# Kernel optimization log

Measured on AMD Instinct MI355X. Metric: run time of the kernel, lower is better.

The kernel has to match this reference:

```python
import jax, jax.numpy as jnp
import numpy as np

HIDDEN = 2048
INTER = 768
NUM_EXPERTS = 32
TOP_K = 4
NUM_TOKENS = 2048


def setup_inputs() -> dict:
    key = jax.random.key(0)
    ks = jax.random.split(key, 5)
    scale = 0.02
    x = jax.random.normal(ks[0], (NUM_TOKENS, HIDDEN), dtype=jnp.float32)
    w_router = jax.random.normal(ks[1], (HIDDEN, NUM_EXPERTS), dtype=jnp.float32) * scale
    w_gate = jax.random.normal(ks[2], (NUM_EXPERTS, HIDDEN, INTER), dtype=jnp.float32) * scale
    w_up = jax.random.normal(ks[3], (NUM_EXPERTS, HIDDEN, INTER), dtype=jnp.float32) * scale
    w_down = jax.random.normal(ks[4], (NUM_EXPERTS, INTER, HIDDEN), dtype=jnp.float32) * scale
    return {"hidden_states": x, "w_router": w_router, "w_gate": w_gate,
            "w_up": w_up, "w_down": w_down}


def reference(hidden_states, w_router, w_gate, w_up, w_down):
    x = hidden_states  # [T, H]
    T = x.shape[0]
    # Router: softmax over experts (in input dtype), top-k, renormalize.
    router_logits = x @ w_router                      # [T, E]
    routing_weights = jax.nn.softmax(router_logits, axis=-1)
    top_w, top_idx = jax.lax.top_k(routing_weights, TOP_K)  # [T, K]
    top_w = top_w / jnp.sum(top_w, axis=-1, keepdims=True)   # norm_topk_prob
    # Dense combine weights: combine[t, e] = routing weight if expert e selected
    # for token t, else 0.  (top-k indices are unique per token.)
    combine = jnp.zeros((T, NUM_EXPERTS), dtype=x.dtype)
    combine = combine.at[jnp.arange(T)[:, None], top_idx].add(top_w)  # [T, E]

    # Scan over experts: each step computes one expert's SwiGLU MLP on all
    # tokens and accumulates it weighted by its combine weight (tokens with
    # zero weight contribute nothing, matching the gather/scatter original).
    def body(acc, expert):
        wg, wu, wd, cw = expert  # [H,I], [H,I], [I,H], [T]
        h = jax.nn.silu(x @ wg) * (x @ wu)   # [T, I]
        return acc + (h @ wd) * cw[:, None], None

    out, _ = jax.lax.scan(body, jnp.zeros_like(x),
                          (w_gate, w_up, w_down, combine.T))
    return out
```

## Files before the change

kernel.cpp:

```cpp
#include <hip/hip_runtime.h>

#define T_TOK 2048
#define HID   2048
#define INTER 768
#define NE    32
#define NSLOT 8192
#define MAXT  96

typedef short bf16x8 __attribute__((ext_vector_type(8)));
typedef float f32x4  __attribute__((ext_vector_type(4)));

__device__ __forceinline__ unsigned short f2b(float f){
  unsigned u = __builtin_bit_cast(unsigned, f);
  u += 0x7fffu + ((u >> 16) & 1u);
  return (unsigned short)(u >> 16);
}
__device__ __forceinline__ unsigned pk2(float a, float b){
  return (unsigned)f2b(a) | ((unsigned)f2b(b) << 16);
}

#define XB_OFF    0ul
#define HBUF_OFF  8388608ul
#define TKW_OFF   20971520ul
#define TKI_OFF   21004288ul
#define ROWS_OFF  21037056ul
#define WTS_OFF   21069824ul
#define OFFS_OFF  21102592ul
#define LOGIT_OFF 21102848ul
#define CNT_OFF   21364992ul
#define FILL_OFF  21365120ul
#define TLIST_OFF 21365248ul
#define ZERO_OFF  21102848ul
#define ZERO_SZ   (262144ul + 128ul + 128ul)

__global__ void convert_x_kernel(const float* __restrict__ x, ushort* __restrict__ xb){
  int i = (blockIdx.x * 256 + threadIdx.x) * 8;
  float4 a = *(const float4*)(x + i);
  float4 b = *(const float4*)(x + i + 4);
  uint4 o;
  o.x = pk2(a.x, a.y);
  o.y = pk2(a.z, a.w);
  o.z = pk2(b.x, b.y);
  o.w = pk2(b.z, b.w);
  *(uint4*)(xb + i) = o;
}

__global__ void router_gemm(const float* __restrict__ x, const float* __restrict__ wr,
                            float* __restrict__ logits){
  const int tt = blockIdx.x;
  const int kb = blockIdx.y;
  __shared__ float xs[64 * 64];
  __shared__ float wsm[64 * 32];
  const int tid = threadIdx.x;
  const int r = tid >> 5, e = tid & 31;
  float acc[8];
#pragma unroll
  for (int i = 0; i < 8; i++) acc[i] = 0.0f;

  for (int sub = 0; sub < 4; ++sub){
    const int k0 = kb * 256 + sub * 64;
    __syncthreads();
#pragma unroll
    for (int j = 0; j < 4; j++){
      int f4 = tid + j * 256;
      int row = f4 >> 4, c4 = f4 & 15;
      float4 v = *(const float4*)(x + (size_t)(tt * 64 + row) * HID + k0 + c4 * 4);
      *(float4*)(xs + row * 64 + c4 * 4) = v;
    }
#pragma unroll
    for (int j = 0; j < 2; j++){
      int f4 = tid + j * 256;
      int row = f4 >> 3, c4 = f4 & 7;
      float4 v = *(const float4*)(wr + (size_t)(k0 + row) * NE + c4 * 4);
      *(float4*)(wsm + row * NE + c4 * 4) = v;
    }
    __syncthreads();
    for (int kk = 0; kk < 64; kk++){
      float wv = wsm[kk * NE + e];
#pragma unroll
      for (int i = 0; i < 8; i++) acc[i] += xs[(r + i * 8) * 64 + kk] * wv;
    }
  }
#pragma unroll
  for (int i = 0; i < 8; i++)
    atomicAdd(&logits[(size_t)(tt * 64 + r + i * 8) * NE + e], acc[i]);
}

__global__ void topk_kernel(const float* __restrict__ logits, float* __restrict__ topk_w,
                            int* __restrict__ topk_i, int* __restrict__ counts){
  int t = blockIdx.x * blockDim.x + threadIdx.x;
  if (t >= T_TOK) return;
  float l[32];
  const float4* lp = (const float4*)(logits + (size_t)t * NE);
#pragma unroll
  for (int i = 0; i < 8; i++){
    float4 v = lp[i];
    l[i*4+0] = v.x; l[i*4+1] = v.y; l[i*4+2] = v.z; l[i*4+3] = v.w;
  }
  float m = l[0];
#pragma unroll
  for (int i = 1; i < 32; i++) m = fmaxf(m, l[i]);
#pragma unroll
  for (int i = 0; i < 32; i++) l[i] = __expf(l[i] - m);
  float wsel[4]; int isel[4];
#pragma unroll
  for (int k = 0; k < 4; k++){
    float best = l[0]; int bi = 0;
#pragma unroll
    for (int i = 1; i < 32; i++){ if (l[i] > best){ best = l[i]; bi = i; } }
    wsel[k] = best; isel[k] = bi; l[bi] = -1.0f;
  }
  float s4 = wsel[0] + wsel[1] + wsel[2] + wsel[3];
  float inv = 1.0f / s4;
#pragma unroll
  for (int k = 0; k < 4; k++){
    topk_w[t * 4 + k] = wsel[k] * inv;
    topk_i[t * 4 + k] = isel[k];
    atomicAdd(&counts[isel[k]], 1);
  }
}

__global__ void prefix_kernel(const int* __restrict__ counts, int* __restrict__ offsets,
                              int* __restrict__ tlist){
  if (threadIdx.x == 0){
    int a = 0; offsets[0] = 0; int nt_ = 0;
    for (int e = 0; e < NE; e++){
      int c = counts[e];
      for (int m = 0; m * 128 < c && nt_ < MAXT; m++) tlist[nt_++] = e | (m << 16);
      a += c; offsets[e + 1] = a;
    }
    for (; nt_ < MAXT; nt_++) tlist[nt_] = -1;
  }
}

__global__ void scatter_kernel(const int* __restrict__ topk_i, const float* __restrict__ topk_w,
                               const int* __restrict__ offsets, int* __restrict__ fill,
                               int* __restrict__ rows, float* __restrict__ wts){
  int gid = blockIdx.x * 256 + threadIdx.x;
  int t = gid >> 2;
  int e = topk_i[gid];
  int pos = atomicAdd(&fill[e], 1);
  int s = offsets[e] + pos;
  rows[s] = t;
  wts[s] = topk_w[gid];
}

#define NT_GU 32
__global__ __launch_bounds__(512, 2) void gateup_kernel(
    const ushort* __restrict__ xb, const float* __restrict__ wg,
    const float* __restrict__ wu, const int* __restrict__ rows,
    const float* __restrict__ wts, const int* __restrict__ counts,
    const int* __restrict__ offsets, const int* __restrict__ tlist,
    ushort* __restrict__ hbuf)
{
  const int w = tlist[blockIdx.y];
  if (w < 0) return;
  const int e = w & 0xffff, mt = w >> 16;
  const int nt = blockIdx.x;
  const int cnt = counts[e];
  const int off = offsets[e];
  const int n0 = nt * 64;

  __shared__ __align__(16) ushort lds[2 * 16384];

  const int tid = threadIdx.x;

  const int ra = tid >> 2, quad = tid & 3;
  const int srow = mt * 128 + ra;
  const int slotA = off + (srow < cnt ? srow : 0);
  const int tokA = rows[slotA];
  const ushort* agp = xb + (size_t)tokA * HID;
  const int q0 = quad * 2, q1 = q0 + 1;
  const int axk = ra & 7;
  const int adst0 = ra * 64 + (q0 ^ axk) * 8;
  const int adst1 = ra * 64 + (q1 ^ axk) * 8;

  const int bn = tid & 63, kg = tid >> 6;
  const size_t wofs = (size_t)e * (HID * INTER) + n0 + bn;
  const float* wgp = wg + wofs;
  const float* wup = wu + wofs;
  const int bdst = bn * 64 + (kg ^ (bn & 7)) * 8;

  const int lane = tid & 63, wv = tid >> 6;
  const int wm = wv >> 1, wn = wv & 1;
  const int fr = lane & 15, ko = lane >> 4;
  const int fxk = fr & 7;

  f32x4 accg[2][2], accu[2][2];
#pragma unroll
  for (int i = 0; i < 2; i++)
#pragma unroll
    for (int j = 0; j < 2; j++){ accg[i][j] = (f32x4)(0.0f); accu[i][j] = (f32x4)(0.0f); }

  uint4 pa0, pa1;
  float sg[8], su[8];

  pa0 = *(const uint4*)(agp + q0 * 8);
  pa1 = *(const uint4*)(agp + q1 * 8);
  {
    const float* pg_ = wgp + (size_t)(kg * 8) * INTER;
    const float* pu_ = wup + (size_t)(kg * 8) * INTER;
#pragma unroll
    for (int kk = 0; kk < 8; kk++){ sg[kk] = pg_[(size_t)kk * INTER]; su[kk] = pu_[(size_t)kk * INTER]; }
  }
  {
    ushort* dA = lds;
    *(uint4*)(dA + adst0) = pa0;
    *(uint4*)(dA + adst1) = pa1;
    uint4 pg, pu;
    pg.x = pk2(sg[0], sg[1]); pg.y = pk2(sg[2], sg[3]);
    pg.z = pk2(sg[4], sg[5]); pg.w = pk2(sg[6], sg[7]);
    pu.x = pk2(su[0], su[1]); pu.y = pk2(su[2], su[3]);
    pu.z = pk2(su[4], su[5]); pu.w = pk2(su[6], su[7]);
    *(uint4*)(dA + 8192 + bdst) = pg;
    *(uint4*)(dA + 12288 + bdst) = pu;
  }
  __syncthreads();

  int cbase = 0;
  for (int t = 0; t < NT_GU; ++t){
    const int nb = cbase ^ 16384;
    if (t + 1 < NT_GU){
      const int k0 = (t + 1) * 64;
      pa0 = *(const uint4*)(agp + k0 + q0 * 8);
      pa1 = *(const uint4*)(agp + k0 + q1 * 8);
      const float* pg_ = wgp + (size_t)(k0 + kg * 8) * INTER;
      const float* pu_ = wup + (size_t)(k0 + kg * 8) * INTER;
#pragma unroll
      for (int kk = 0; kk < 8; kk++){ sg[kk] = pg_[(size_t)kk * INTER]; su[kk] = pu_[(size_t)kk * INTER]; }
    }
    const ushort* A  = lds + cbase;
    const ushort* BG = lds + cbase + 8192;
    const ushort* BU = lds + cbase + 12288;
#pragma unroll
    for (int kk = 0; kk < 2; kk++){
      const int bsel = ((kk * 4 + ko) ^ fxk) * 8;
      bf16x8 a[2], bg2[2], bu2[2];
#pragma unroll
      for (int mf = 0; mf < 2; mf++)
        a[mf] = *(const bf16x8*)(A + (wm * 32 + mf * 16 + fr) * 64 + bsel);
#pragma unroll
      for (int nf = 0; nf < 2; nf++){
        bg2[nf] = *(const bf16x8*)(BG + (wn * 32 + nf * 16 + fr) * 64 + bsel);
        bu2[nf] = *(const bf16x8*)(BU + (wn * 32 + nf * 16 + fr) * 64 + bsel);
      }
#pragma unroll
      for (int mf = 0; mf < 2; mf++)
#pragma unroll
        for (int nf = 0; nf < 2; nf++){
          accg[mf][nf] = __builtin_amdgcn_mfma_f32_16x16x32_bf16(a[mf], bg2[nf], accg[mf][nf], 0, 0, 0);
          accu[mf][nf] = __builtin_amdgcn_mfma_f32_16x16x32_bf16(a[mf], bu2[nf], accu[mf][nf], 0, 0, 0);
        }
    }
    if (t + 1 < NT_GU){
      ushort* dA = lds + nb;
      *(uint4*)(dA + adst0) = pa0;
      *(uint4*)(dA + adst1) = pa1;
      uint4 pg, pu;
      pg.x = pk2(sg[0], sg[1]); pg.y = pk2(sg[2], sg[3]);
      pg.z = pk2(sg[4], sg[5]); pg.w = pk2(sg[6], sg[7]);
      pu.x = pk2(su[0], su[1]); pu.y = pk2(su[2], su[3]);
      pu.z = pk2(su[4], su[5]); pu.w = pk2(su[6], su[7]);
      *(uint4*)(dA + 8192 + bdst) = pg;
      *(uint4*)(dA + 12288 + bdst) = pu;
    }
    __syncthreads();
    cbase = nb;
  }

#pragma unroll
  for (int mf = 0; mf < 2; mf++)
#pragma unroll
    for (int j = 0; j < 4; j++){
      int rl = wm * 32 + mf * 16 + ko * 4 + j;
      int gr = mt * 128 + rl;
      if (gr < cnt){
        float w2 = wts[off + gr];
        size_t robase = (size_t)(off + gr) * INTER + n0;
#pragma unroll
        for (int nf = 0; nf < 2; nf++){
          float g = accg[mf][nf][j], u = accu[mf][nf][j];
          float h = (g / (1.0f + __expf(-g))) * u * w2;
          hbuf[robase + wn * 32 + nf * 16 + fr] = f2b(h);
        }
      }
    }
}

#define NT_DN 12
__global__ __launch_bounds__(512, 2) void down_kernel(
    const ushort* __restrict__ hbuf, const float* __restrict__ wd,
    const int* __restrict__ rows, const int* __restrict__ counts,
    const int* __restrict__ offsets, const int* __restrict__ tlist,
    float* __restrict__ out)
{
  const int w = tlist[blockIdx.y];
  if (w < 0) return;
  const int e = w & 0xffff, mt = w >> 16;
  const int nt = blockIdx.x;
  const int cnt = counts[e];
  const int off = offsets[e];
  const int n0 = nt * 64;

  __shared__ __align__(16) ushort lds[2 * 12288];

  const int tid = threadIdx.x;

  const int ra = tid >> 2, quad = tid & 3;
  const int srow = mt * 128 + ra;
  const int slotA = off + (srow < cnt ? srow : 0);
  const ushort* agp = hbuf + (size_t)slotA * INTER;
  const int q0 = quad * 2, q1 = q0 + 1;
  const int axk = ra & 7;
  const int adst0 = ra * 64 + (q0 ^ axk) * 8;
  const int adst1 = ra * 64 + (q1 ^ axk) * 8;

  const int bn = tid & 63, kg = tid >> 6;
  const float* wdp = wd + (size_t)e * (INTER * HID) + n0 + bn;
  const int bdst = bn * 64 + (kg ^ (bn & 7)) * 8;

  const int lane = tid & 63, wv = tid >> 6;
  const int wm = wv >> 1, wn = wv & 1;
  const int fr = lane & 15, ko = lane >> 4;
  const int fxk = fr & 7;

  f32x4 acc[2][2];
#pragma unroll
  for (int i = 0; i < 2; i++)
#pragma unroll
    for (int j = 0; j < 2; j++) acc[i][j] = (f32x4)(0.0f);

  uint4 pa0, pa1;
  float sb[8];

  pa0 = *(const uint4*)(agp + q0 * 8);
  pa1 = *(const uint4*)(agp + q1 * 8);
  {
    const float* p = wdp + (size_t)(kg * 8) * HID;
#pragma unroll
    for (int kk = 0; kk < 8; kk++) sb[kk] = p[(size_t)kk * HID];
  }
  {
    ushort* dA = lds;
    *(uint4*)(dA + adst0) = pa0;
    *(uint4*)(dA + adst1) = pa1;
    uint4 pb;
    pb.x = pk2(sb[0], sb[1]); pb.y = pk2(sb[2], sb[3]);
    pb.z = pk2(sb[4], sb[5]); pb.w = pk2(sb[6], sb[7]);
    *(uint4*)(dA + 8192 + bdst) = pb;
  }
  __syncthreads();

  int cbase = 0;
  for (int t = 0; t < NT_DN; ++t){
    const int nb = cbase ^ 12288;
    if (t + 1 < NT_DN){
      const int k0 = (t + 1) * 64;
      pa0 = *(const uint4*)(agp + k0 + q0 * 8);
      pa1 = *(const uint4*)(agp + k0 + q1 * 8);
      const float* p = wdp + (size_t)(k0 + kg * 8) * HID;
#pragma unroll
      for (int kk = 0; kk < 8; kk++) sb[kk] = p[(size_t)kk * HID];
    }
    const ushort* A = lds + cbase;
    const ushort* B = lds + cbase + 8192;
#pragma unroll
    for (int kk = 0; kk < 2; kk++){
      const int bsel = ((kk * 4 + ko) ^ fxk) * 8;
      bf16x8 a[2], b2[2];
#pragma unroll
      for (int mf = 0; mf < 2; mf++)
        a[mf] = *(const bf16x8*)(A + (wm * 32 + mf * 16 + fr) * 64 + bsel);
#pragma unroll
      for (int nf = 0; nf < 2; nf++)
        b2[nf] = *(const bf16x8*)(B + (wn * 32 + nf * 16 + fr) * 64 + bsel);
#pragma unroll
      for (int mf = 0; mf < 2; mf++)
#pragma unroll
        for (int nf = 0; nf < 2; nf++)
          acc[mf][nf] = __builtin_amdgcn_mfma_f32_16x16x32_bf16(a[mf], b2[nf], acc[mf][nf], 0, 0, 0);
    }
    if (t + 1 < NT_DN){
      ushort* dA = lds + nb;
      *(uint4*)(dA + adst0) = pa0;
      *(uint4*)(dA + adst1) = pa1;
      uint4 pb;
      pb.x = pk2(sb[0], sb[1]); pb.y = pk2(sb[2], sb[3]);
      pb.z = pk2(sb[4], sb[5]); pb.w = pk2(sb[6], sb[7]);
      *(uint4*)(dA + 8192 + bdst) = pb;
    }
    __syncthreads();
    cbase = nb;
  }

#pragma unroll
  for (int mf = 0; mf < 2; mf++)
#pragma unroll
    for (int j = 0; j < 4; j++){
      int rl = wm * 32 + mf * 16 + ko * 4 + j;
      int gr = mt * 128 + rl;
      if (gr < cnt){
        int tok = rows[off + gr];
        float* obase = out + (size_t)tok * HID + n0;
#pragma unroll
        for (int nf = 0; nf < 2; nf++)
          atomicAdd(obase + wn * 32 + nf * 16 + fr, acc[mf][nf][j]);
      }
    }
}

extern "C" void kernel_launch(void* const* d_in, const int* in_sizes, int n_in,
                              void* d_out, int out_size, void* d_ws, size_t ws_size,
                              hipStream_t stream){
  const float* x  = (const float*)d_in[0];
  const float* wr = (const float*)d_in[1];
  const float* wg = (const float*)d_in[2];
  const float* wu = (const float*)d_in[3];
  const float* wd = (const float*)d_in[4];
  float* out = (float*)d_out;
  char* ws = (char*)d_ws;

  ushort* xb     = (ushort*)(ws + XB_OFF);
  ushort* hbuf   = (ushort*)(ws + HBUF_OFF);
  float*  topkw  = (float*)(ws + TKW_OFF);
  int*    topki  = (int*)(ws + TKI_OFF);
  int*    rows   = (int*)(ws + ROWS_OFF);
  float*  wts    = (float*)(ws + WTS_OFF);
  int*    offs   = (int*)(ws + OFFS_OFF);
  float*  logits = (float*)(ws + LOGIT_OFF);
  int*    counts = (int*)(ws + CNT_OFF);
  int*    fill   = (int*)(ws + FILL_OFF);
  int*    tlist  = (int*)(ws + TLIST_OFF);

  hipMemsetAsync(ws + ZERO_OFF, 0, ZERO_SZ, stream);
  hipMemsetAsync(d_out, 0, (size_t)out_size * sizeof(float), stream);

  convert_x_kernel<<<2048, 256, 0, stream>>>(x, xb);
  router_gemm<<<dim3(32, 8), 256, 0, stream>>>(x, wr, logits);
  topk_kernel<<<8, 256, 0, stream>>>(logits, topkw, topki, counts);
  prefix_kernel<<<1, 64, 0, stream>>>(counts, offs, tlist);
  scatter_kernel<<<32, 256, 0, stream>>>(topki, topkw, offs, fill, rows, wts);
  gateup_kernel<<<dim3(12, MAXT), 512, 0, stream>>>(xb, wg, wu, rows, wts, counts, offs, tlist, hbuf);
  down_kernel<<<dim3(32, MAXT), 512, 0, stream>>>(hbuf, wd, rows, counts, offs, tlist, out);
}
```

Before: 347.7 us.

## Deepen prefetch, swap grid order, replace output atomics with slot buffer plus combine

Both GEMM kernels now hold two register prefetch sets, unrolling the double-buffered loop by two so global loads run two tiles ahead. The launch-bounds occupancy hint rises from 2 to 4 and the grid axes are swapped so the expert/m-tile index varies fastest. When the workspace is large enough, the down projection writes per-slot fp32 rows instead of atomically adding into the output, and a new combine kernel sums each token's four slots. This removes atomics and the output memset at the cost of a 64MB intermediate buffer and extra memory traffic, and the tighter register budget risks spills.

```diff
diff --git a/kernel.cpp b/kernel.cpp
--- a/kernel.cpp
+++ b/kernel.cpp
@@ -30,6 +30,9 @@
 #define CNT_OFF   21364992ul
 #define FILL_OFF  21365120ul
 #define TLIST_OFF 21365248ul
+#define T2S_OFF   21365760ul
+#define HB2_OFF   21398528ul
+#define WS_NEED   (HB2_OFF + 67108864ul)
 #define ZERO_OFF  21102848ul
 #define ZERO_SZ   (262144ul + 128ul + 128ul)
 
@@ -135,7 +138,8 @@
 
 __global__ void scatter_kernel(const int* __restrict__ topk_i, const float* __restrict__ topk_w,
                                const int* __restrict__ offsets, int* __restrict__ fill,
-                               int* __restrict__ rows, float* __restrict__ wts){
+                               int* __restrict__ rows, float* __restrict__ wts,
+                               int* __restrict__ t2s){
   int gid = blockIdx.x * 256 + threadIdx.x;
   int t = gid >> 2;
   int e = topk_i[gid];
@@ -143,20 +147,21 @@
   int s = offsets[e] + pos;
   rows[s] = t;
   wts[s] = topk_w[gid];
+  t2s[gid] = s;
 }
 
 #define NT_GU 32
-__global__ __launch_bounds__(512, 2) void gateup_kernel(
+__global__ __launch_bounds__(512, 4) void gateup_kernel(
     const ushort* __restrict__ xb, const float* __restrict__ wg,
     const float* __restrict__ wu, const int* __restrict__ rows,
     const float* __restrict__ wts, const int* __restrict__ counts,
     const int* __restrict__ offsets, const int* __restrict__ tlist,
     ushort* __restrict__ hbuf)
 {
-  const int w = tlist[blockIdx.y];
+  const int w = tlist[blockIdx.x];
   if (w < 0) return;
   const int e = w & 0xffff, mt = w >> 16;
-  const int nt = blockIdx.x;
+  const int nt = blockIdx.y;
   const int cnt = counts[e];
   const int off = offsets[e];
   const int n0 = nt * 64;
@@ -192,46 +197,33 @@
 #pragma unroll
     for (int j = 0; j < 2; j++){ accg[i][j] = (f32x4)(0.0f); accu[i][j] = (f32x4)(0.0f); }
 
-  uint4 pa0, pa1;
-  float sg[8], su[8];
-
-  pa0 = *(const uint4*)(agp + q0 * 8);
-  pa1 = *(const uint4*)(agp + q1 * 8);
-  {
-    const float* pg_ = wgp + (size_t)(kg * 8) * INTER;
-    const float* pu_ = wup + (size_t)(kg * 8) * INTER;
-#pragma unroll
-    for (int kk = 0; kk < 8; kk++){ sg[kk] = pg_[(size_t)kk * INTER]; su[kk] = pu_[(size_t)kk * INTER]; }
-  }
-  {
-    ushort* dA = lds;
-    *(uint4*)(dA + adst0) = pa0;
-    *(uint4*)(dA + adst1) = pa1;
+  uint4 A0a, A0b, A1a, A1b;
+  float G0[8], U0[8], G1[8], U1[8];
+
+  auto loadSet = [&](int k0, uint4 &aa, uint4 &ab, float *g, float *u){
+    aa = *(const uint4*)(agp + k0 + q0 * 8);
+    ab = *(const uint4*)(agp + k0 + q1 * 8);
+    const float* pg_ = wgp + (size_t)(k0 + kg * 8) * INTER;
+    const float* pu_ = wup + (size_t)(k0 + kg * 8) * INTER;
+#pragma unroll
+    for (int kk = 0; kk < 8; kk++){ g[kk] = pg_[(size_t)kk * INTER]; u[kk] = pu_[(size_t)kk * INTER]; }
+  };
+  auto writeSet = [&](int base, uint4 aa, uint4 ab, const float *g, const float *u){
+    ushort* dA = lds + base;
+    *(uint4*)(dA + adst0) = aa;
+    *(uint4*)(dA + adst1) = ab;
     uint4 pg, pu;
-    pg.x = pk2(sg[0], sg[1]); pg.y = pk2(sg[2], sg[3]);
-    pg.z = pk2(sg[4], sg[5]); pg.w = pk2(sg[6], sg[7]);
-    pu.x = pk2(su[0], su[1]); pu.y = pk2(su[2], su[3]);
-    pu.z = pk2(su[4], su[5]); pu.w = pk2(su[6], su[7]);
+    pg.x = pk2(g[0], g[1]); pg.y = pk2(g[2], g[3]);
+    pg.z = pk2(g[4], g[5]); pg.w = pk2(g[6], g[7]);
+    pu.x = pk2(u[0], u[1]); pu.y = pk2(u[2], u[3]);
+    pu.z = pk2(u[4], u[5]); pu.w = pk2(u[6], u[7]);
     *(uint4*)(dA + 8192 + bdst) = pg;
     *(uint4*)(dA + 12288 + bdst) = pu;
-  }
-  __syncthreads();
-
-  int cbase = 0;
-  for (int t = 0; t < NT_GU; ++t){
-    const int nb = cbase ^ 16384;
-    if (t + 1 < NT_GU){
-      const int k0 = (t + 1) * 64;
-      pa0 = *(const uint4*)(agp + k0 + q0 * 8);
-      pa1 = *(const uint4*)(agp + k0 + q1 * 8);
-      const float* pg_ = wgp + (size_t)(k0 + kg * 8) * INTER;
-      const float* pu_ = wup + (size_t)(k0 + kg * 8) * INTER;
-#pragma unroll
-      for (int kk = 0; kk < 8; kk++){ sg[kk] = pg_[(size_t)kk * INTER]; su[kk] = pu_[(size_t)kk * INTER]; }
-    }
-    const ushort* A  = lds + cbase;
-    const ushort* BG = lds + cbase + 8192;
-    const ushort* BU = lds + cbase + 12288;
+  };
+  auto computeTile = [&](int base){
+    const ushort* A  = lds + base;
+    const ushort* BG = lds + base + 8192;
+    const ushort* BU = lds + base + 12288;
 #pragma unroll
     for (int kk = 0; kk < 2; kk++){
       const int bsel = ((kk * 4 + ko) ^ fxk) * 8;
@@ -252,20 +244,22 @@
           accu[mf][nf] = __builtin_amdgcn_mfma_f32_16x16x32_bf16(a[mf], bu2[nf], accu[mf][nf], 0, 0, 0);
         }
     }
-    if (t + 1 < NT_GU){
-      ushort* dA = lds + nb;
-      *(uint4*)(dA + adst0) = pa0;
-      *(uint4*)(dA + adst1) = pa1;
-      uint4 pg, pu;
-      pg.x = pk2(sg[0], sg[1]); pg.y = pk2(sg[2], sg[3]);
-      pg.z = pk2(sg[4], sg[5]); pg.w = pk2(sg[6], sg[7]);
-      pu.x = pk2(su[0], su[1]); pu.y = pk2(su[2], su[3]);
-      pu.z = pk2(su[4], su[5]); pu.w = pk2(su[6], su[7]);
-      *(uint4*)(dA + 8192 + bdst) = pg;
-      *(uint4*)(dA + 12288 + bdst) = pu;
-    }
-    __syncthreads();
-    cbase = nb;
+  };
+
+  loadSet(0,  A0a, A0b, G0, U0);
+  loadSet(64, A1a, A1b, G1, U1);
+  writeSet(0, A0a, A0b, G0, U0);
+  __syncthreads();
+
+  for (int t = 0; t < NT_GU; t += 2){
+    if (t + 2 < NT_GU) loadSet((t + 2) * 64, A0a, A0b, G0, U0);
+    computeTile(0);
+    writeSet(16384, A1a, A1b, G1, U1);
+    __syncthreads();
+    if (t + 3 < NT_GU) loadSet((t + 3) * 64, A1a, A1b, G1, U1);
+    computeTile(16384);
+    if (t + 2 < NT_GU) writeSet(0, A0a, A0b, G0, U0);
+    __syncthreads();
   }
 
 #pragma unroll
@@ -288,16 +282,17 @@
 }
 
 #define NT_DN 12
-__global__ __launch_bounds__(512, 2) void down_kernel(
+template<bool SLOT>
+__global__ __launch_bounds__(512, 4) void down_kernel(
     const ushort* __restrict__ hbuf, const float* __restrict__ wd,
     const int* __restrict__ rows, const int* __restrict__ counts,
     const int* __restrict__ offsets, const int* __restrict__ tlist,
-    float* __restrict__ out)
+    float* __restrict__ outp)
 {
-  const int w = tlist[blockIdx.y];
+  const int w = tlist[blockIdx.x];
   if (w < 0) return;
   const int e = w & 0xffff, mt = w >> 16;
-  const int nt = blockIdx.x;
+  const int nt = blockIdx.y;
   const int cnt = counts[e];
   const int off = offsets[e];
   const int n0 = nt * 64;
@@ -330,40 +325,28 @@
 #pragma unroll
     for (int j = 0; j < 2; j++) acc[i][j] = (f32x4)(0.0f);
 
-  uint4 pa0, pa1;
-  float sb[8];
-
-  pa0 = *(const uint4*)(agp + q0 * 8);
-  pa1 = *(const uint4*)(agp + q1 * 8);
-  {
-    const float* p = wdp + (size_t)(kg * 8) * HID;
-#pragma unroll
-    for (int kk = 0; kk < 8; kk++) sb[kk] = p[(size_t)kk * HID];
-  }
-  {
-    ushort* dA = lds;
-    *(uint4*)(dA + adst0) = pa0;
-    *(uint4*)(dA + adst1) = pa1;
+  uint4 A0a, A0b, A1a, A1b;
+  float B0[8], B1[8];
+
+  auto loadSet = [&](int k0, uint4 &aa, uint4 &ab, float *b){
+    aa = *(const uint4*)(agp + k0 + q0 * 8);
+    ab = *(const uint4*)(agp + k0 + q1 * 8);
+    const float* p = wdp + (size_t)(k0 + kg * 8) * HID;
+#pragma unroll
+    for (int kk = 0; kk < 8; kk++) b[kk] = p[(size_t)kk * HID];
+  };
+  auto writeSet = [&](int base, uint4 aa, uint4 ab, const float *b){
+    ushort* dA = lds + base;
+    *(uint4*)(dA + adst0) = aa;
+    *(uint4*)(dA + adst1) = ab;
     uint4 pb;
-    pb.x = pk2(sb[0], sb[1]); pb.y = pk2(sb[2], sb[3]);
-    pb.z = pk2(sb[4], sb[5]); pb.w = pk2(sb[6], sb[7]);
+    pb.x = pk2(b[0], b[1]); pb.y = pk2(b[2], b[3]);
+    pb.z = pk2(b[4], b[5]); pb.w = pk2(b[6], b[7]);
     *(uint4*)(dA + 8192 + bdst) = pb;
-  }
-  __syncthreads();
-
-  int cbase = 0;
-  for (int t = 0; t < NT_DN; ++t){
-    const int nb = cbase ^ 12288;
-    if (t + 1 < NT_DN){
-      const int k0 = (t + 1) * 64;
-      pa0 = *(const uint4*)(agp + k0 + q0 * 8);
-      pa1 = *(const uint4*)(agp + k0 + q1 * 8);
-      const float* p = wdp + (size_t)(k0 + kg * 8) * HID;
-#pragma unroll
-      for (int kk = 0; kk < 8; kk++) sb[kk] = p[(size_t)kk * HID];
-    }
-    const ushort* A = lds + cbase;
-    const ushort* B = lds + cbase + 8192;
+  };
+  auto computeTile = [&](int base){
+    const ushort* A = lds + base;
+    const ushort* B = lds + base + 8192;
 #pragma unroll
     for (int kk = 0; kk < 2; kk++){
       const int bsel = ((kk * 4 + ko) ^ fxk) * 8;
@@ -380,17 +363,22 @@
         for (int nf = 0; nf < 2; nf++)
           acc[mf][nf] = __builtin_amdgcn_mfma_f32_16x16x32_bf16(a[mf], b2[nf], acc[mf][nf], 0, 0, 0);
     }
-    if (t + 1 < NT_DN){
-      ushort* dA = lds + nb;
-      *(uint4*)(dA + adst0) = pa0;
-      *(uint4*)(dA + adst1) = pa1;
-      uint4 pb;
-      pb.x = pk2(sb[0], sb[1]); pb.y = pk2(sb[2], sb[3]);
-      pb.z = pk2(sb[4], sb[5]); pb.w = pk2(sb[6], sb[7]);
-      *(uint4*)(dA + 8192 + bdst) = pb;
-    }
-    __syncthreads();
-    cbase = nb;
+  };
+
+  loadSet(0,  A0a, A0b, B0);
+  loadSet(64, A1a, A1b, B1);
+  writeSet(0, A0a, A0b, B0);
+  __syncthreads();
+
+  for (int t = 0; t < NT_DN; t += 2){
+    if (t + 2 < NT_DN) loadSet((t + 2) * 64, A0a, A0b, B0);
+    computeTile(0);
+    writeSet(12288, A1a, A1b, B1);
+    __syncthreads();
+    if (t + 3 < NT_DN) loadSet((t + 3) * 64, A1a, A1b, B1);
+    computeTile(12288);
+    if (t + 2 < NT_DN) writeSet(0, A0a, A0b, B0);
+    __syncthreads();
   }
 
 #pragma unroll
@@ -400,13 +388,38 @@
       int rl = wm * 32 + mf * 16 + ko * 4 + j;
       int gr = mt * 128 + rl;
       if (gr < cnt){
-        int tok = rows[off + gr];
-        float* obase = out + (size_t)tok * HID + n0;
-#pragma unroll
-        for (int nf = 0; nf < 2; nf++)
-          atomicAdd(obase + wn * 32 + nf * 16 + fr, acc[mf][nf][j]);
+        if (SLOT){
+          float* obase = outp + (size_t)(off + gr) * HID + n0;
+#pragma unroll
+          for (int nf = 0; nf < 2; nf++)
+            obase[wn * 32 + nf * 16 + fr] = acc[mf][nf][j];
+        } else {
+          int tok = rows[off + gr];
+          float* obase = outp + (size_t)tok * HID + n0;
+#pragma unroll
+          for (int nf = 0; nf < 2; nf++)
+            atomicAdd(obase + wn * 32 + nf * 16 + fr, acc[mf][nf][j]);
+        }
       }
     }
+}
+
+__global__ void combine_kernel(const float* __restrict__ hbuf2, const int* __restrict__ t2s,
+                               float* __restrict__ out){
+  const int t = blockIdx.y;
+  const int c4 = (blockIdx.x * 256 + threadIdx.x) * 4;
+  const int s0 = t2s[t * 4 + 0], s1 = t2s[t * 4 + 1];
+  const int s2 = t2s[t * 4 + 2], s3 = t2s[t * 4 + 3];
+  float4 a = *(const float4*)(hbuf2 + (size_t)s0 * HID + c4);
+  float4 b = *(const float4*)(hbuf2 + (size_t)s1 * HID + c4);
+  float4 c = *(const float4*)(hbuf2 + (size_t)s2 * HID + c4);
+  float4 d = *(const float4*)(hbuf2 + (size_t)s3 * HID + c4);
+  float4 r;
+  r.x = a.x + b.x + c.x + d.x;
+  r.y = a.y + b.y + c.y + d.y;
+  r.z = a.z + b.z + c.z + d.z;
+  r.w = a.w + b.w + c.w + d.w;
+  *(float4*)(out + (size_t)t * HID + c4) = r;
 }
 
 extern "C" void kernel_launch(void* const* d_in, const int* in_sizes, int n_in,
@@ -431,15 +444,24 @@
   int*    counts = (int*)(ws + CNT_OFF);
   int*    fill   = (int*)(ws + FILL_OFF);
   int*    tlist  = (int*)(ws + TLIST_OFF);
+  int*    t2s    = (int*)(ws + T2S_OFF);
+  float*  hbuf2  = (float*)(ws + HB2_OFF);
+
+  const bool slotpath = (ws_size >= WS_NEED);
 
   hipMemsetAsync(ws + ZERO_OFF, 0, ZERO_SZ, stream);
-  hipMemsetAsync(d_out, 0, (size_t)out_size * sizeof(float), stream);
 
   convert_x_kernel<<<2048, 256, 0, stream>>>(x, xb);
   router_gemm<<<dim3(32, 8), 256, 0, stream>>>(x, wr, logits);
   topk_kernel<<<8, 256, 0, stream>>>(logits, topkw, topki, counts);
   prefix_kernel<<<1, 64, 0, stream>>>(counts, offs, tlist);
-  scatter_kernel<<<32, 256, 0, stream>>>(topki, topkw, offs, fill, rows, wts);
-  gateup_kernel<<<dim3(12, MAXT), 512, 0, stream>>>(xb, wg, wu, rows, wts, counts, offs, tlist, hbuf);
-  down_kernel<<<dim3(32, MAXT), 512, 0, stream>>>(hbuf, wd, rows, counts, offs, tlist, out);
-}
+  scatter_kernel<<<32, 256, 0, stream>>>(topki, topkw, offs, fill, rows, wts, t2s);
+  gateup_kernel<<<dim3(MAXT, 12), 512, 0, stream>>>(xb, wg, wu, rows, wts, counts, offs, tlist, hbuf);
+  if (slotpath){
+    down_kernel<true><<<dim3(MAXT, 32), 512, 0, stream>>>(hbuf, wd, rows, counts, offs, tlist, hbuf2);
+    combine_kernel<<<dim3(2, T_TOK), 256, 0, stream>>>(hbuf2, t2s, out);
+  } else {
+    hipMemsetAsync(d_out, 0, (size_t)out_size * sizeof(float), stream);
+    down_kernel<false><<<dim3(MAXT, 32), 512, 0, stream>>>(hbuf, wd, rows, counts, offs, tlist, out);
+  }
+}
```

Result: slower. 885.7 us (+154.7%).
